# Performance work log

Measured on AMD Instinct MI355X. Metric: run time of the kernel, lower is better.

## Reference

```python
import jax, jax.numpy as jnp
import numpy as np

B, N, F, U = 16, 2048, 64, 64

def setup_inputs() -> dict:
    key = jax.random.key(0)
    k1, k2, k3 = jax.random.split(key, 3)
    node_features = jax.random.normal(k1, (B, N, F), dtype=jnp.float32)
    adjacency_matrix = (jax.random.uniform(k2, (B, N, N)) < 0.01).astype(jnp.float32)
    kernel = jax.random.normal(k3, (F, U), dtype=jnp.float32) * (1.0 / np.sqrt(F))
    return {"node_features": node_features, "adjacency_matrix": adjacency_matrix, "kernel": kernel}

def reference(node_features, adjacency_matrix, kernel):
    # A_tilde = A + I  (self-loops)
    n = adjacency_matrix.shape[-1]
    adj = adjacency_matrix + jnp.eye(n, dtype=adjacency_matrix.dtype)
    # symmetric normalization D^-1/2 A_tilde D^-1/2 (diag matmuls == broadcast scaling)
    row_sum = jnp.sum(adj, axis=-1)                      # [B, N]
    d_inv_sqrt = jnp.where(row_sum > 0, row_sum ** -0.5, 0.0)
    norm_adj = d_inv_sqrt[:, :, None] * adj * d_inv_sqrt[:, None, :]
    # feature transform then aggregate, fused with ReLU
    transformed = jnp.einsum('bnf,fu->bnu', node_features, kernel)
    out = jnp.einsum('bnm,bmu->bnu', norm_adj, transformed)
    return jax.nn.relu(out)
```

## Files before the change

kernel.cpp:

```cpp
#include <hip/hip_runtime.h>
#include <hip/hip_bf16.h>


#define NB     16
#define NN     2048
#define NF     64
#define NU     64
#define NROWS  (NB * NN)
#define NGRP   (NROWS / 4)
#define NBLK   2048
#define K12IT  (NGRP / NBLK)

typedef unsigned int uint;
typedef uint vuint4 __attribute__((ext_vector_type(4)));

__device__ __forceinline__ int map_row(int g, int wid) {
    const int x = g & 7, s = g >> 3;
    const int batch = x + ((s >> 9) << 3);
    const int grp = s & 511;
    return (batch << 11) + (grp << 2) + wid;
}

__global__ __launch_bounds__(256) void k12_scan_transform(
    const float* __restrict__ X, const float* __restrict__ A,
    const float* __restrict__ W, float* __restrict__ Tp,
    float* __restrict__ d, int* __restrict__ counts,
    int* __restrict__ idx, int cap)
{
    __shared__ float sW[NF * NU];
    const int t = threadIdx.x, wid = t >> 6, lane = t & 63;
    #pragma unroll
    for (int k = 0; k < 4; ++k)
        reinterpret_cast<float4*>(sW)[t + 256 * k] =
            reinterpret_cast<const float4*>(W)[t + 256 * k];
    __syncthreads();

    const unsigned long long lmask_lt = (lane == 63) ? 0x7fffffffffffffffull
                                                     : ((1ull << lane) - 1ull);
    for (int it = 0; it < K12IT; ++it) {
        const int g   = blockIdx.x + it * NBLK;
        const int row = map_row(g, wid);

        const float xv = X[(size_t)row * NF + lane];
        const uint* Arow = reinterpret_cast<const uint*>(A + (size_t)row * NN);
        vuint4 a[8];
        #pragma unroll
        for (int c = 0; c < 8; ++c)
            a[c] = __builtin_nontemporal_load(
                reinterpret_cast<const vuint4*>(Arow) + c * 64 + lane);

        float acc = 0.f;
        #pragma unroll
        for (int f = 0; f < NF; ++f)
            acc += __shfl(xv, f) * sW[f * NU + lane];

        const size_t base = (size_t)row * cap;
        int cnt = 0;
        #pragma unroll
        for (int c = 0; c < 8; ++c) {
            #pragma unroll
            for (int e = 0; e < 4; ++e) {
                const bool nz = (a[c][e] != 0u);
                const unsigned long long m = __ballot(nz);
                if (m) {
                    if (nz) {
                        const int slot = cnt + __popcll(m & lmask_lt);
                        if (slot < cap)
                            idx[base + slot] = ((c * 64 + lane) << 2) + e;
                    }
                    cnt += __popcll(m);
                }
            }
        }

        const float di = rsqrtf((float)cnt + 1.0f);
        if (lane == 0) { d[row] = di; counts[row] = cnt; }
        Tp[(size_t)row * NU + lane] = acc * di;
    }
}

__global__ __launch_bounds__(256) void k3_aggregate(
    const float* __restrict__ A, const float* __restrict__ Tp,
    const float* __restrict__ d, const int* __restrict__ counts,
    const int* __restrict__ idx, float* __restrict__ out, int cap)
{
    const int t = threadIdx.x, wid = t >> 6, lane = t & 63;
    const int row = map_row(blockIdx.x, wid);
    const int b   = row >> 11;
    const float* Tb = Tp + (((size_t)b) << 11) * NU;

    float a0 = Tp[(size_t)row * NU + lane];
    float a1 = 0.f;
    const int cnt = counts[row];
    if (cnt <= cap) {
        const size_t base = (size_t)row * cap;
        const int4* q4 = reinterpret_cast<const int4*>(idx + base);
        const int nfull = cnt >> 2;
        for (int q = 0; q < nfull; ++q) {
            const int4 qq = q4[q];
            const float t0 = Tb[((size_t)(uint)qq.x << 6) + lane];
            const float t1 = Tb[((size_t)(uint)qq.y << 6) + lane];
            const float t2 = Tb[((size_t)(uint)qq.z << 6) + lane];
            const float t3 = Tb[((size_t)(uint)qq.w << 6) + lane];
            a0 += t0 + t2;
            a1 += t1 + t3;
        }
        for (int k = nfull << 2; k < cnt; ++k)
            a1 += Tb[((size_t)(uint)idx[base + k] << 6) + lane];
    } else {
        const float* Arow = A + (size_t)row * NN;
        for (int j = 0; j < NN; ++j)
            if (Arow[j] != 0.f) a1 += Tb[((size_t)j << 6) + lane];
    }
    const float r = d[row] * (a0 + a1);
    out[(size_t)row * NU + lane] = r > 0.f ? r : 0.f;
}

extern "C" void kernel_launch(void* const* d_in, const int* in_sizes, int n_in,
                              void* d_out, int out_size, void* d_ws, size_t ws_size,
                              hipStream_t stream)
{
    const float* X = (const float*)d_in[0];
    const float* A = (const float*)d_in[1];
    const float* W = (const float*)d_in[2];
    float* out = (float*)d_out;

    char* ws = (char*)d_ws;
    float* Tp     = (float*)ws;
    float* dvec   = (float*)(ws + (size_t)NROWS * NU * 4);
    int*   counts = (int*)  (ws + (size_t)NROWS * NU * 4 + (size_t)NROWS * 4);
    int*   idx    = (int*)  (ws + (size_t)NROWS * NU * 4 + 2ull * NROWS * 4);

    const size_t fixed = (size_t)NROWS * NU * 4 + 2ull * NROWS * 4;
    int cap = 0;
    if (ws_size > fixed) {
        size_t c = (ws_size - fixed) / ((size_t)NROWS * sizeof(int));
        cap = (int)(c < 128 ? c : 128);
        cap &= ~3;
    }

    k12_scan_transform<<<NBLK, 256, 0, stream>>>(X, A, W, Tp, dvec, counts, idx, cap);
    k3_aggregate<<<NGRP, 256, 0, stream>>>(A, Tp, dvec, counts, idx, out, cap);
}
```

Before: 420.3 us.

## Launch one block per row group, keep W column in registers, pipeline gather indices

The scan/transform kernel drops its persistent grid-stride loop and launches one block per group of four rows. Each lane now holds its W column in 64 registers, read straight from global memory instead of from shared memory, and broadcasts x with readlane. The aggregate kernel prefetches the next two int4 index chunks and splits the sum across four accumulators for more memory-level parallelism, and the output uses nontemporal stores. The risks are higher register pressure from the wcol array, which could lower occupancy, and re-reading W from global memory in every block.

```diff
diff --git a/kernel.cpp b/kernel.cpp
--- a/kernel.cpp
+++ b/kernel.cpp
@@ -8,8 +8,6 @@
 #define NU     64
 #define NROWS  (NB * NN)
 #define NGRP   (NROWS / 4)
-#define NBLK   2048
-#define K12IT  (NGRP / NBLK)
 
 typedef unsigned int uint;
 typedef uint vuint4 __attribute__((ext_vector_type(4)));
@@ -27,56 +25,53 @@
     float* __restrict__ d, int* __restrict__ counts,
     int* __restrict__ idx, int cap)
 {
-    __shared__ float sW[NF * NU];
     const int t = threadIdx.x, wid = t >> 6, lane = t & 63;
+    const int row = map_row(blockIdx.x, wid);
+
+    float wcol[NF];
     #pragma unroll
-    for (int k = 0; k < 4; ++k)
-        reinterpret_cast<float4*>(sW)[t + 256 * k] =
-            reinterpret_cast<const float4*>(W)[t + 256 * k];
-    __syncthreads();
+    for (int f = 0; f < NF; ++f) wcol[f] = W[f * NU + lane];
+    const float xv = X[(size_t)row * NF + lane];
+
+    const uint* Arow = reinterpret_cast<const uint*>(A + (size_t)row * NN);
+    vuint4 a[8];
+    #pragma unroll
+    for (int c = 0; c < 8; ++c)
+        a[c] = __builtin_nontemporal_load(
+            reinterpret_cast<const vuint4*>(Arow) + c * 64 + lane);
+
+    float acc = 0.f;
+    #pragma unroll
+    for (int f = 0; f < NF; ++f) {
+        const float xf = __int_as_float(
+            __builtin_amdgcn_readlane(__float_as_int(xv), f));
+        acc += xf * wcol[f];
+    }
 
     const unsigned long long lmask_lt = (lane == 63) ? 0x7fffffffffffffffull
                                                      : ((1ull << lane) - 1ull);
-    for (int it = 0; it < K12IT; ++it) {
-        const int g   = blockIdx.x + it * NBLK;
-        const int row = map_row(g, wid);
-
-        const float xv = X[(size_t)row * NF + lane];
-        const uint* Arow = reinterpret_cast<const uint*>(A + (size_t)row * NN);
-        vuint4 a[8];
+    const size_t base = (size_t)row * cap;
+    int cnt = 0;
+    #pragma unroll
+    for (int c = 0; c < 8; ++c) {
         #pragma unroll
-        for (int c = 0; c < 8; ++c)
-            a[c] = __builtin_nontemporal_load(
-                reinterpret_cast<const vuint4*>(Arow) + c * 64 + lane);
-
-        float acc = 0.f;
-        #pragma unroll
-        for (int f = 0; f < NF; ++f)
-            acc += __shfl(xv, f) * sW[f * NU + lane];
-
-        const size_t base = (size_t)row * cap;
-        int cnt = 0;
-        #pragma unroll
-        for (int c = 0; c < 8; ++c) {
-            #pragma unroll
-            for (int e = 0; e < 4; ++e) {
-                const bool nz = (a[c][e] != 0u);
-                const unsigned long long m = __ballot(nz);
-                if (m) {
-                    if (nz) {
-                        const int slot = cnt + __popcll(m & lmask_lt);
-                        if (slot < cap)
-                            idx[base + slot] = ((c * 64 + lane) << 2) + e;
-                    }
-                    cnt += __popcll(m);
+        for (int e = 0; e < 4; ++e) {
+            const bool nz = (a[c][e] != 0u);
+            const unsigned long long m = __ballot(nz);
+            if (m) {
+                if (nz) {
+                    const int slot = cnt + __popcll(m & lmask_lt);
+                    if (slot < cap)
+                        idx[base + slot] = ((c * 64 + lane) << 2) + e;
                 }
+                cnt += __popcll(m);
             }
         }
+    }
 
-        const float di = rsqrtf((float)cnt + 1.0f);
-        if (lane == 0) { d[row] = di; counts[row] = cnt; }
-        Tp[(size_t)row * NU + lane] = acc * di;
-    }
+    const float di = rsqrtf((float)cnt + 1.0f);
+    if (lane == 0) { d[row] = di; counts[row] = cnt; }
+    Tp[(size_t)row * NU + lane] = acc * di;
 }
 
 __global__ __launch_bounds__(256) void k3_aggregate(
@@ -90,20 +85,34 @@
     const float* Tb = Tp + (((size_t)b) << 11) * NU;
 
     float a0 = Tp[(size_t)row * NU + lane];
-    float a1 = 0.f;
+    float a1 = 0.f, a2 = 0.f, a3 = 0.f;
     const int cnt = counts[row];
     if (cnt <= cap) {
         const size_t base = (size_t)row * cap;
         const int4* q4 = reinterpret_cast<const int4*>(idx + base);
         const int nfull = cnt >> 2;
-        for (int q = 0; q < nfull; ++q) {
-            const int4 qq = q4[q];
-            const float t0 = Tb[((size_t)(uint)qq.x << 6) + lane];
-            const float t1 = Tb[((size_t)(uint)qq.y << 6) + lane];
-            const float t2 = Tb[((size_t)(uint)qq.z << 6) + lane];
-            const float t3 = Tb[((size_t)(uint)qq.w << 6) + lane];
-            a0 += t0 + t2;
-            a1 += t1 + t3;
+        int q = 0;
+        int4 qa, qb;
+        if (nfull > 0) qa = q4[0];
+        if (nfull > 1) qb = q4[1];
+        for (; q + 2 <= nfull; q += 2) {
+            const int4 c0 = qa, c1 = qb;
+            if (q + 2 < nfull) qa = q4[q + 2];
+            if (q + 3 < nfull) qb = q4[q + 3];
+            a0 += Tb[((size_t)(uint)c0.x << 6) + lane];
+            a1 += Tb[((size_t)(uint)c0.y << 6) + lane];
+            a2 += Tb[((size_t)(uint)c0.z << 6) + lane];
+            a3 += Tb[((size_t)(uint)c0.w << 6) + lane];
+            a0 += Tb[((size_t)(uint)c1.x << 6) + lane];
+            a1 += Tb[((size_t)(uint)c1.y << 6) + lane];
+            a2 += Tb[((size_t)(uint)c1.z << 6) + lane];
+            a3 += Tb[((size_t)(uint)c1.w << 6) + lane];
+        }
+        if (q < nfull) {
+            a0 += Tb[((size_t)(uint)qa.x << 6) + lane];
+            a1 += Tb[((size_t)(uint)qa.y << 6) + lane];
+            a2 += Tb[((size_t)(uint)qa.z << 6) + lane];
+            a3 += Tb[((size_t)(uint)qa.w << 6) + lane];
         }
         for (int k = nfull << 2; k < cnt; ++k)
             a1 += Tb[((size_t)(uint)idx[base + k] << 6) + lane];
@@ -112,8 +121,9 @@
         for (int j = 0; j < NN; ++j)
             if (Arow[j] != 0.f) a1 += Tb[((size_t)j << 6) + lane];
     }
-    const float r = d[row] * (a0 + a1);
-    out[(size_t)row * NU + lane] = r > 0.f ? r : 0.f;
+    const float r = d[row] * ((a0 + a1) + (a2 + a3));
+    __builtin_nontemporal_store(r > 0.f ? r : 0.f,
+                                &out[(size_t)row * NU + lane]);
 }
 
 extern "C" void kernel_launch(void* const* d_in, const int* in_sizes, int n_in,
@@ -139,6 +149,6 @@
         cap &= ~3;
     }
 
-    k12_scan_transform<<<NBLK, 256, 0, stream>>>(X, A, W, Tp, dvec, counts, idx, cap);
+    k12_scan_transform<<<NGRP, 256, 0, stream>>>(X, A, W, Tp, dvec, counts, idx, cap);
     k3_aggregate<<<NGRP, 256, 0, stream>>>(A, Tp, dvec, counts, idx, out, cap);
 }
```

After: 381.1 us. 1.1x faster.
